# Performance work log

Measured on AMD Instinct MI355X. Metric: run time of the kernel, lower is better.

## Reference

```python
import jax, jax.numpy as jnp
import numpy as np

SCALE = 0.5

def setup_inputs() -> dict:
    key = jax.random.key(0)
    kx, kw, kb = jax.random.split(key, 3)
    N, Cin, H, W = 32, 64, 128, 128
    Cout, K = 128, 3
    x = jax.random.normal(kx, (N, Cin, H, W), dtype=jnp.float32)
    # kaiming_uniform with a=sqrt(5) -> bound = sqrt(3/fan_in) approx; uniform is fine for a reference
    fan_in = Cin * K * K
    bound = 1.0 / np.sqrt(fan_in)
    weight = jax.random.uniform(kw, (Cout, Cin, K, K), dtype=jnp.float32, minval=-bound, maxval=bound)
    bias = jax.random.uniform(kb, (Cout,), dtype=jnp.float32, minval=-bound, maxval=bound)
    return {"x": x, "weight": weight, "bias": bias}

def reference(x, weight, bias):
    # valid conv, stride 1: (N, Cout, OH, OW)
    y = jax.lax.conv_general_dilated(
        x, weight,
        window_strides=(1, 1),
        padding="VALID",
        dimension_numbers=("NCHW", "OIHW", "NCHW"),
    )
    y = (y + bias[None, :, None, None]) * SCALE
    # min over output channels, keepdim -> (N, 1, OH, OW)
    return jnp.min(y, axis=1, keepdims=True)
```

## Files before the change

kernel.cpp:

```cpp
#include <hip/hip_runtime.h>

constexpr int CN   = 32;
constexpr int CIN  = 64;
constexpr int CH   = 128;
constexpr int CW   = 128;
constexpr int COUT = 128;
constexpr int OHh  = 126;
constexpr int OWw  = 126;
constexpr int KTOT = 576;

typedef __attribute__((ext_vector_type(8))) short bf16x8;
typedef __attribute__((ext_vector_type(4))) float f32x4;

__device__ __forceinline__ unsigned short f2bf(float f) {
  union { float f; unsigned u; } v; v.f = f;
  unsigned u = v.u;
  u += 0x7FFFu + ((u >> 16) & 1u);
  return (unsigned short)(u >> 16);
}

__device__ __forceinline__ void gload_lds16(const unsigned short* g, unsigned short* l) {
  __builtin_amdgcn_global_load_lds(
      (const __attribute__((address_space(1))) unsigned int*)g,
      (__attribute__((address_space(3))) unsigned int*)l, 16, 0, 0);
}

__global__ __launch_bounds__(256) void prep_xt_kernel(const float* __restrict__ x,
                                                      unsigned short* __restrict__ xt) {
  __shared__ __align__(16) unsigned short s[128][72];
  const int b = blockIdx.x;
  const int n = b >> 7, h = b & 127;
  const float* src = x + (size_t)n * CIN * CH * CW + (size_t)h * CW;
  const int t = threadIdx.x;
  #pragma unroll
  for (int r = 0; r < 8; ++r) {
    int idx = r * 256 + t;
    int ci = idx >> 5, c0 = (idx & 31) << 2;
    float4 v = *(const float4*)(src + (size_t)ci * (CH * CW) + c0);
    s[c0 + 0][ci] = f2bf(v.x);
    s[c0 + 1][ci] = f2bf(v.y);
    s[c0 + 2][ci] = f2bf(v.z);
    s[c0 + 3][ci] = f2bf(v.w);
  }
  __syncthreads();
  unsigned short* dst = xt + (size_t)b * 8192;
  #pragma unroll
  for (int r = 0; r < 4; ++r) {
    int idx = r * 256 + t;
    int c = idx >> 3, sl = idx & 7;
    int half = sl >> 2, q = sl & 3;
    int lo = q ^ ((c >> 1) & 3);
    uint4 v = *(const uint4*)&s[c][half * 32 + lo * 8];
    *(uint4*)(dst + (size_t)c * 64 + sl * 8) = v;
  }
}

__global__ void prep_wt3_kernel(const float* __restrict__ w,
                                unsigned short* __restrict__ wt3) {
  int e = blockIdx.x * 256 + threadIdx.x;
  if (e >= COUT * KTOT) return;
  int j = e & 7, lane = (e >> 3) & 63, mi = (e >> 9) & 3, wc = (e >> 11) & 1;
  int p = e >> 12;
  int G = p / 3, kw = p - G * 3;
  int kh = G >> 1, half = G & 1;
  int co = wc * 64 + mi * 16 + (lane & 15);
  int ci = half * 32 + (lane >> 4) * 8 + j;
  wt3[e] = f2bf(w[co * 576 + ci * 9 + kh * 3 + kw]);
}

__global__ __launch_bounds__(512, 4)
void conv_min_mfma6(const unsigned short* __restrict__ xt,
                    const unsigned short* __restrict__ wt3,
                    const float* __restrict__ bias,
                    float* __restrict__ out) {
  __shared__ __align__(16) unsigned short sX[2][2][130][32];
  __shared__ float sRed[2][256];

  const int t   = threadIdx.x;
  const int bid = blockIdx.x;
  const int swz = (bid & 7) * 252 + (bid >> 3);
  const int n   = swz / 63;
  const int oh0 = (swz - n * 63) * 2;

  const int lane = t & 63, w = t >> 6;
  const int wc = w & 1;
  const int wr = (w >> 1) & 1;
  const int wh = w >> 2;
  const int lg = lane >> 4, ln = lane & 15;

  const int xcq = (t >> 2) * 64 + (t & 3) * 8;

  const char* Bb[3];
  #pragma unroll
  for (int kw = 0; kw < 3; ++kw) {
    int row = wh * 64 + ln + kw;
    int ch = lg ^ ((row >> 1) & 3);
    Bb[kw] = (const char*)&sX[0][0][0][0] + wr * 8320 + row * 64 + ch * 16;
  }
  const unsigned short* wlane = wt3 + wc * 2048 + lane * 8;

  f32x4 acc[4][4];
  #pragma unroll
  for (int i = 0; i < 4; ++i)
    #pragma unroll
    for (int j = 0; j < 4; ++j)
      acc[i][j] = (f32x4){0.f, 0.f, 0.f, 0.f};

  auto stageX = [&](int G, int buf) {
    #pragma unroll
    for (int r = 0; r < 2; ++r) {
      int h = oh0 + (G >> 1) + r;
      gload_lds16(xt + ((size_t)(n * 128 + h) << 13) + (G & 1) * 32 + xcq,
                  &sX[buf][r][0][0] + w * 512);
    }
  };

  stageX(0, 0);

  #pragma unroll
  for (int p = 0; p < 18; ++p) {
    const int G = p / 3, kw = p - G * 3, buf = G & 1;
    if (kw == 0) {
      asm volatile("s_waitcnt vmcnt(0)" ::: "memory");
      __builtin_amdgcn_s_barrier();
      if (G < 5) stageX(G + 1, buf ^ 1);
    }
    bf16x8 af[4], bfr[4];
    #pragma unroll
    for (int mi = 0; mi < 4; ++mi)
      af[mi] = *(const bf16x8*)(wlane + p * 4096 + mi * 512);
    #pragma unroll
    for (int ni = 0; ni < 4; ++ni)
      bfr[ni] = *(const bf16x8*)(Bb[kw] + buf * 16640 + ni * 1024);
    __builtin_amdgcn_s_setprio(1);
    #pragma unroll
    for (int mi = 0; mi < 4; ++mi)
      #pragma unroll
      for (int ni = 0; ni < 4; ++ni)
        acc[mi][ni] = __builtin_amdgcn_mfma_f32_16x16x32_bf16(
            af[mi], bfr[ni], acc[mi][ni], 0, 0, 0);
    __builtin_amdgcn_s_setprio(0);
  }

  float bv[4][4];
  #pragma unroll
  for (int mi = 0; mi < 4; ++mi)
    #pragma unroll
    for (int r = 0; r < 4; ++r)
      bv[mi][r] = bias[wc * 64 + mi * 16 + lg * 4 + r];

  #pragma unroll
  for (int ni = 0; ni < 4; ++ni) {
    float m = 3.4e38f;
    #pragma unroll
    for (int mi = 0; mi < 4; ++mi)
      #pragma unroll
      for (int r = 0; r < 4; ++r)
        m = fminf(m, (acc[mi][ni][r] + bv[mi][r]) * 0.5f);
    m = fminf(m, __shfl_xor(m, 16));
    m = fminf(m, __shfl_xor(m, 32));
    if (lg == 0) sRed[wc][wr * 128 + wh * 64 + ni * 16 + ln] = m;
  }
  __syncthreads();
  if (t < 256) {
    int row = t >> 7, c = t & 127;
    if (c < OWw)
      out[((size_t)n * OHh + oh0 + row) * OWw + c] = fminf(sRed[0][t], sRed[1][t]);
  }
}

__global__ void prep_wt_kernel(const float* __restrict__ w,
                               unsigned short* __restrict__ wt) {
  int i = blockIdx.x * 256 + threadIdx.x;
  if (i >= COUT * KTOT) return;
  int co = i / KTOT, kp = i - co * KTOT;
  int kw = kp / 192, rem = kp - kw * 192;
  int ci = rem / 3, kh = rem - ci * 3;
  wt[i] = f2bf(w[co * 576 + ci * 9 + kh * 3 + kw]);
}

template <bool USE_WT>
__global__ __launch_bounds__(256, 2)
void conv_min_fb(const float* __restrict__ x, const float* __restrict__ w,
                 const float* __restrict__ bias, const unsigned short* __restrict__ wt,
                 float* __restrict__ out) {
  __shared__ __align__(16) unsigned short sW[128][40];
  __shared__ __align__(16) unsigned short sX[128][40];
  __shared__ float sBias[COUT];
  __shared__ float sRed[2][128];
  const int t = threadIdx.x, bid = blockIdx.x;
  const int n = bid / OHh, oh = bid - n * OHh;
  if (t < COUT) sBias[t] = bias[t];
  const int hq = t & 7, q = t >> 3, c0 = q * 4;
  const int wco = t >> 1, whalf = t & 1;
  const int lane = t & 63, lg = lane >> 4, ln = lane & 15;
  const int wv = t >> 6, wc = wv & 1, wp = wv >> 1;
  f32x4 acc[4][4];
  #pragma unroll
  for (int i = 0; i < 4; ++i)
    #pragma unroll
    for (int j = 0; j < 4; ++j) acc[i][j] = (f32x4){0.f, 0.f, 0.f, 0.f};
  const float* xn = x + (size_t)n * CIN * CH * CW;
  for (int s = 0; s < 18; ++s) {
    const int k0 = s * 32;
    const int kw_s = s / 6;
    const int rembase = (s - kw_s * 6) * 32;
    float4 xa[2], xb[2]; int kkp[2];
    #pragma unroll
    for (int pi = 0; pi < 2; ++pi) {
      const int kk = 2 * hq + 16 * pi; kkp[pi] = kk;
      int rem0 = rembase + kk, ci0 = rem0 / 3, kh0 = rem0 - ci0 * 3;
      int rem1 = rem0 + 1, ci1 = rem1 / 3, kh1 = rem1 - ci1 * 3;
      xa[pi] = *(const float4*)(xn + (ci0 * CH + (oh + kh0)) * CW + c0);
      xb[pi] = *(const float4*)(xn + (ci1 * CH + (oh + kh1)) * CW + c0);
    }
    uint4 wv0, wv1;
    if constexpr (USE_WT) {
      const uint4* src = (const uint4*)(wt + wco * KTOT + k0 + whalf * 16);
      wv0 = src[0]; wv1 = src[1];
    } else {
      unsigned tmp[8];
      #pragma unroll
      for (int e = 0; e < 8; ++e) {
        int kk = whalf * 16 + 2 * e;
        int rem0 = rembase + kk, ci0 = rem0 / 3, kh0 = rem0 - ci0 * 3;
        int rem1 = rem0 + 1, ci1 = rem1 / 3, kh1 = rem1 - ci1 * 3;
        tmp[e] = (unsigned)f2bf(w[wco * 576 + ci0 * 9 + kh0 * 3 + kw_s]) |
                 ((unsigned)f2bf(w[wco * 576 + ci1 * 9 + kh1 * 3 + kw_s]) << 16);
      }
      wv0 = make_uint4(tmp[0], tmp[1], tmp[2], tmp[3]);
      wv1 = make_uint4(tmp[4], tmp[5], tmp[6], tmp[7]);
    }
    __syncthreads();
    #pragma unroll
    for (int pi = 0; pi < 2; ++pi)
      #pragma unroll
      for (int j = 0; j < 4; ++j) {
        int p = c0 + j - kw_s;
        unsigned pk = (unsigned)f2bf(((const float*)&xa[pi])[j]) |
                      ((unsigned)f2bf(((const float*)&xb[pi])[j]) << 16);
        if (p >= 0) *(unsigned*)&sX[p][kkp[pi]] = pk;
      }
    *(uint4*)&sW[wco][whalf * 16] = wv0;
    *(uint4*)&sW[wco][whalf * 16 + 8] = wv1;
    __syncthreads();
    bf16x8 af[4], bfr[4];
    #pragma unroll
    for (int mi = 0; mi < 4; ++mi) af[mi] = *(const bf16x8*)&sW[wc * 64 + mi * 16 + ln][lg * 8];
    #pragma unroll
    for (int ni = 0; ni < 4; ++ni) bfr[ni] = *(const bf16x8*)&sX[wp * 64 + ni * 16 + ln][lg * 8];
    #pragma unroll
    for (int mi = 0; mi < 4; ++mi)
      #pragma unroll
      for (int ni = 0; ni < 4; ++ni)
        acc[mi][ni] = __builtin_amdgcn_mfma_f32_16x16x32_bf16(af[mi], bfr[ni], acc[mi][ni], 0, 0, 0);
  }
  #pragma unroll
  for (int ni = 0; ni < 4; ++ni) {
    float m = 3.4e38f;
    #pragma unroll
    for (int mi = 0; mi < 4; ++mi)
      #pragma unroll
      for (int r = 0; r < 4; ++r)
        m = fminf(m, (acc[mi][ni][r] + sBias[wc * 64 + mi * 16 + lg * 4 + r]) * 0.5f);
    m = fminf(m, __shfl_xor(m, 16));
    m = fminf(m, __shfl_xor(m, 32));
    if (lg == 0) sRed[wc][wp * 64 + ni * 16 + ln] = m;
  }
  __syncthreads();
  if (t < OWw) out[(size_t)(n * OHh + oh) * OWw + t] = fminf(sRed[0][t], sRed[1][t]);
}

extern "C" void kernel_launch(void* const* d_in, const int* in_sizes, int n_in,
                              void* d_out, int out_size, void* d_ws, size_t ws_size,
                              hipStream_t stream) {
  const float* x    = (const float*)d_in[0];
  const float* w    = (const float*)d_in[1];
  const float* bias = (const float*)d_in[2];
  float* out = (float*)d_out;

  const size_t XT_BYTES = (size_t)CN * CH * CW * CIN * 2;
  const size_t WT_BYTES = (size_t)COUT * KTOT * 2;

  if (d_ws && ws_size >= XT_BYTES + WT_BYTES) {
    unsigned short* xt  = (unsigned short*)d_ws;
    unsigned short* wt3 = (unsigned short*)((char*)d_ws + XT_BYTES);
    prep_xt_kernel<<<CN * CH, 256, 0, stream>>>(x, xt);
    prep_wt3_kernel<<<(COUT * KTOT + 255) / 256, 256, 0, stream>>>(w, wt3);
    conv_min_mfma6<<<2016, 512, 0, stream>>>(xt, wt3, bias, out);
  } else if (d_ws && ws_size >= WT_BYTES) {
    unsigned short* wt = (unsigned short*)d_ws;
    prep_wt_kernel<<<(COUT * KTOT + 255) / 256, 256, 0, stream>>>(w, wt);
    conv_min_fb<true><<<CN * OHh, 256, 0, stream>>>(x, w, bias, wt, out);
  } else {
    conv_min_fb<false><<<CN * OHh, 256, 0, stream>>>(x, w, bias, nullptr, out);
  }
}
```

Baseline: 104.1 us.

## Fuse input bf16 transpose into conv kernel via register-staged prefetch

```diff
diff --git a/kernel.cpp b/kernel.cpp
--- a/kernel.cpp
+++ b/kernel.cpp
@@ -1,4 +1,5 @@
 #include <hip/hip_runtime.h>
+#include <hip/hip_bf16.h>
 
 constexpr int CN   = 32;
 constexpr int CIN  = 64;
@@ -19,40 +20,10 @@
   return (unsigned short)(u >> 16);
 }
 
-__device__ __forceinline__ void gload_lds16(const unsigned short* g, unsigned short* l) {
-  __builtin_amdgcn_global_load_lds(
-      (const __attribute__((address_space(1))) unsigned int*)g,
-      (__attribute__((address_space(3))) unsigned int*)l, 16, 0, 0);
-}
-
-__global__ __launch_bounds__(256) void prep_xt_kernel(const float* __restrict__ x,
-                                                      unsigned short* __restrict__ xt) {
-  __shared__ __align__(16) unsigned short s[128][72];
-  const int b = blockIdx.x;
-  const int n = b >> 7, h = b & 127;
-  const float* src = x + (size_t)n * CIN * CH * CW + (size_t)h * CW;
-  const int t = threadIdx.x;
-  #pragma unroll
-  for (int r = 0; r < 8; ++r) {
-    int idx = r * 256 + t;
-    int ci = idx >> 5, c0 = (idx & 31) << 2;
-    float4 v = *(const float4*)(src + (size_t)ci * (CH * CW) + c0);
-    s[c0 + 0][ci] = f2bf(v.x);
-    s[c0 + 1][ci] = f2bf(v.y);
-    s[c0 + 2][ci] = f2bf(v.z);
-    s[c0 + 3][ci] = f2bf(v.w);
-  }
-  __syncthreads();
-  unsigned short* dst = xt + (size_t)b * 8192;
-  #pragma unroll
-  for (int r = 0; r < 4; ++r) {
-    int idx = r * 256 + t;
-    int c = idx >> 3, sl = idx & 7;
-    int half = sl >> 2, q = sl & 3;
-    int lo = q ^ ((c >> 1) & 3);
-    uint4 v = *(const uint4*)&s[c][half * 32 + lo * 8];
-    *(uint4*)(dst + (size_t)c * 64 + sl * 8) = v;
-  }
+__device__ __forceinline__ unsigned packbf2(float a, float b) {
+  union { __hip_bfloat162 h; unsigned u; } v;
+  v.h = __float22bfloat162_rn(make_float2(a, b));
+  return v.u;
 }
 
 __global__ void prep_wt3_kernel(const float* __restrict__ w,
@@ -69,7 +40,7 @@
 }
 
 __global__ __launch_bounds__(512, 4)
-void conv_min_mfma6(const unsigned short* __restrict__ xt,
+void conv_min_mfma7(const float* __restrict__ x,
                     const unsigned short* __restrict__ wt3,
                     const float* __restrict__ bias,
                     float* __restrict__ out) {
@@ -88,7 +59,9 @@
   const int wh = w >> 2;
   const int lg = lane >> 4, ln = lane & 15;
 
-  const int xcq = (t >> 2) * 64 + (t & 3) * 8;
+  const int sr = t >> 8;
+  const int so = (t >> 6) & 3;
+  const int sc = t & 63;
 
   const char* Bb[3];
   #pragma unroll
@@ -106,24 +79,38 @@
     for (int j = 0; j < 4; ++j)
       acc[i][j] = (f32x4){0.f, 0.f, 0.f, 0.f};
 
-  auto stageX = [&](int G, int buf) {
-    #pragma unroll
-    for (int r = 0; r < 2; ++r) {
-      int h = oh0 + (G >> 1) + r;
-      gload_lds16(xt + ((size_t)(n * 128 + h) << 13) + (G & 1) * 32 + xcq,
-                  &sX[buf][r][0][0] + w * 512);
-    }
+  float svA[8], svB[8];
+
+  auto stage_load = [&](int G, float (&sv)[8], int e) {
+    const int h = oh0 + (G >> 1) + sr;
+    const size_t base = ((size_t)((n * 64 + (G & 1) * 32 + so * 8) * 128 + h)) * 128
+                        + sc + e * 64;
+    #pragma unroll
+    for (int j = 0; j < 8; ++j)
+      sv[j] = x[base + (size_t)j * 16384];
   };
-
-  stageX(0, 0);
+  auto stage_write = [&](int G, float (&sv)[8], int e) {
+    const int c = sc + e * 64;
+    const int ch = so ^ ((c >> 1) & 3);
+    uint4 v = make_uint4(packbf2(sv[0], sv[1]), packbf2(sv[2], sv[3]),
+                         packbf2(sv[4], sv[5]), packbf2(sv[6], sv[7]));
+    *(uint4*)(&sX[G & 1][sr][c][ch * 8]) = v;
+  };
+
+  stage_load(0, svA, 0);
+  stage_load(0, svB, 1);
+  stage_write(0, svA, 0);
+  stage_write(0, svB, 1);
+  asm volatile("s_waitcnt lgkmcnt(0)" ::: "memory");
+  __builtin_amdgcn_s_barrier();
+  __builtin_amdgcn_sched_barrier(0);
 
   #pragma unroll
   for (int p = 0; p < 18; ++p) {
     const int G = p / 3, kw = p - G * 3, buf = G & 1;
-    if (kw == 0) {
-      asm volatile("s_waitcnt vmcnt(0)" ::: "memory");
-      __builtin_amdgcn_s_barrier();
-      if (G < 5) stageX(G + 1, buf ^ 1);
+    if (kw == 0 && G < 5) {
+      stage_load(G + 1, svA, 0);
+      __builtin_amdgcn_sched_barrier(0);
     }
     bf16x8 af[4], bfr[4];
     #pragma unroll
@@ -140,6 +127,19 @@
         acc[mi][ni] = __builtin_amdgcn_mfma_f32_16x16x32_bf16(
             af[mi], bfr[ni], acc[mi][ni], 0, 0, 0);
     __builtin_amdgcn_s_setprio(0);
+    if (G < 5) {
+      if (kw == 1) {
+        stage_write(G + 1, svA, 0);
+        stage_load(G + 1, svB, 1);
+      }
+      if (kw == 2) {
+        stage_write(G + 1, svB, 1);
+        asm volatile("s_waitcnt lgkmcnt(0)" ::: "memory");
+        __builtin_amdgcn_sched_barrier(0);
+        __builtin_amdgcn_s_barrier();
+        __builtin_amdgcn_sched_barrier(0);
+      }
+    }
   }
 
   float bv[4][4];
@@ -169,21 +169,9 @@
   }
 }
 
-__global__ void prep_wt_kernel(const float* __restrict__ w,
-                               unsigned short* __restrict__ wt) {
-  int i = blockIdx.x * 256 + threadIdx.x;
-  if (i >= COUT * KTOT) return;
-  int co = i / KTOT, kp = i - co * KTOT;
-  int kw = kp / 192, rem = kp - kw * 192;
-  int ci = rem / 3, kh = rem - ci * 3;
-  wt[i] = f2bf(w[co * 576 + ci * 9 + kh * 3 + kw]);
-}
-
-template <bool USE_WT>
 __global__ __launch_bounds__(256, 2)
 void conv_min_fb(const float* __restrict__ x, const float* __restrict__ w,
-                 const float* __restrict__ bias, const unsigned short* __restrict__ wt,
-                 float* __restrict__ out) {
+                 const float* __restrict__ bias, float* __restrict__ out) {
   __shared__ __align__(16) unsigned short sW[128][40];
   __shared__ __align__(16) unsigned short sX[128][40];
   __shared__ float sBias[COUT];
@@ -202,7 +190,6 @@
     for (int j = 0; j < 4; ++j) acc[i][j] = (f32x4){0.f, 0.f, 0.f, 0.f};
   const float* xn = x + (size_t)n * CIN * CH * CW;
   for (int s = 0; s < 18; ++s) {
-    const int k0 = s * 32;
     const int kw_s = s / 6;
     const int rembase = (s - kw_s * 6) * 32;
     float4 xa[2], xb[2]; int kkp[2];
@@ -214,22 +201,14 @@
       xa[pi] = *(const float4*)(xn + (ci0 * CH + (oh + kh0)) * CW + c0);
       xb[pi] = *(const float4*)(xn + (ci1 * CH + (oh + kh1)) * CW + c0);
     }
-    uint4 wv0, wv1;
-    if constexpr (USE_WT) {
-      const uint4* src = (const uint4*)(wt + wco * KTOT + k0 + whalf * 16);
-      wv0 = src[0]; wv1 = src[1];
-    } else {
-      unsigned tmp[8];
-      #pragma unroll
-      for (int e = 0; e < 8; ++e) {
-        int kk = whalf * 16 + 2 * e;
-        int rem0 = rembase + kk, ci0 = rem0 / 3, kh0 = rem0 - ci0 * 3;
-        int rem1 = rem0 + 1, ci1 = rem1 / 3, kh1 = rem1 - ci1 * 3;
-        tmp[e] = (unsigned)f2bf(w[wco * 576 + ci0 * 9 + kh0 * 3 + kw_s]) |
-                 ((unsigned)f2bf(w[wco * 576 + ci1 * 9 + kh1 * 3 + kw_s]) << 16);
-      }
-      wv0 = make_uint4(tmp[0], tmp[1], tmp[2], tmp[3]);
-      wv1 = make_uint4(tmp[4], tmp[5], tmp[6], tmp[7]);
+    unsigned tmp[8];
+    #pragma unroll
+    for (int e = 0; e < 8; ++e) {
+      int kk = whalf * 16 + 2 * e;
+      int rem0 = rembase + kk, ci0 = rem0 / 3, kh0 = rem0 - ci0 * 3;
+      int rem1 = rem0 + 1, ci1 = rem1 / 3, kh1 = rem1 - ci1 * 3;
+      tmp[e] = (unsigned)f2bf(w[wco * 576 + ci0 * 9 + kh0 * 3 + kw_s]) |
+               ((unsigned)f2bf(w[wco * 576 + ci1 * 9 + kh1 * 3 + kw_s]) << 16);
     }
     __syncthreads();
     #pragma unroll
@@ -241,8 +220,8 @@
                       ((unsigned)f2bf(((const float*)&xb[pi])[j]) << 16);
         if (p >= 0) *(unsigned*)&sX[p][kkp[pi]] = pk;
       }
-    *(uint4*)&sW[wco][whalf * 16] = wv0;
-    *(uint4*)&sW[wco][whalf * 16 + 8] = wv1;
+    *(uint4*)&sW[wco][whalf * 16] = make_uint4(tmp[0], tmp[1], tmp[2], tmp[3]);
+    *(uint4*)&sW[wco][whalf * 16 + 8] = make_uint4(tmp[4], tmp[5], tmp[6], tmp[7]);
     __syncthreads();
     bf16x8 af[4], bfr[4];
     #pragma unroll
@@ -279,20 +258,13 @@
   const float* bias = (const float*)d_in[2];
   float* out = (float*)d_out;
 
-  const size_t XT_BYTES = (size_t)CN * CH * CW * CIN * 2;
   const size_t WT_BYTES = (size_t)COUT * KTOT * 2;
 
-  if (d_ws && ws_size >= XT_BYTES + WT_BYTES) {
-    unsigned short* xt  = (unsigned short*)d_ws;
-    unsigned short* wt3 = (unsigned short*)((char*)d_ws + XT_BYTES);
-    prep_xt_kernel<<<CN * CH, 256, 0, stream>>>(x, xt);
+  if (d_ws && ws_size >= WT_BYTES) {
+    unsigned short* wt3 = (unsigned short*)d_ws;
     prep_wt3_kernel<<<(COUT * KTOT + 255) / 256, 256, 0, stream>>>(w, wt3);
-    conv_min_mfma6<<<2016, 512, 0, stream>>>(xt, wt3, bias, out);
-  } else if (d_ws && ws_size >= WT_BYTES) {
-    unsigned short* wt = (unsigned short*)d_ws;
-    prep_wt_kernel<<<(COUT * KTOT + 255) / 256, 256, 0, stream>>>(w, wt);
-    conv_min_fb<true><<<CN * OHh, 256, 0, stream>>>(x, w, bias, wt, out);
+    conv_min_mfma7<<<2016, 512, 0, stream>>>(x, wt3, bias, out);
   } else {
-    conv_min_fb<false><<<CN * OHh, 256, 0, stream>>>(x, w, bias, nullptr, out);
-  }
-}
+    conv_min_fb<<<CN * OHh, 256, 0, stream>>>(x, w, bias, out);
+  }
+}
```

New measurement: 88.43 us. 1.18x faster.
